# Performance work log

Hardware: AMD Instinct MI355X
Metric: run time of the kernel (lower is better)

The kernel has to match this reference:

```python
import jax, jax.numpy as jnp
import numpy as np

B, S, D, H = 2, 4096, 512, 8
DK = D // H


def setup_inputs() -> dict:
    key = jax.random.key(0)
    ks = jax.random.split(key, 8)
    q = jax.random.normal(ks[0], (B, S, D), dtype=jnp.float32)
    k = jax.random.normal(ks[1], (B, S, D), dtype=jnp.float32)
    v = jax.random.normal(ks[2], (B, S, D), dtype=jnp.float32)
    mask = jax.random.randint(ks[3], (B, S, S), 0, 2, dtype=jnp.int32)
    scale = 1.0 / np.sqrt(D)
    w_q = jax.random.normal(ks[4], (D, D), dtype=jnp.float32) * scale
    w_k = jax.random.normal(ks[5], (D, D), dtype=jnp.float32) * scale
    w_v = jax.random.normal(ks[6], (D, D), dtype=jnp.float32) * scale
    w_o = jax.random.normal(ks[7], (D, D), dtype=jnp.float32) * scale
    return {"q": q, "k": k, "v": v, "mask": mask,
            "w_q": w_q, "w_k": w_k, "w_v": w_v, "w_o": w_o}


def reference(q, k, v, mask, w_q, w_k, w_v, w_o):
    # Projections (weights stored as [in, out]; no bias, matching bias=False)
    # [B,S,D] -> [B,H,S,DK]
    def split_heads(x):
        return x.reshape(B, S, H, DK).transpose(0, 2, 1, 3)

    qh = split_heads(q @ w_q)
    kh = split_heads(k @ w_k)
    vh = split_heads(v @ w_v)

    inv_sqrt_dk = jnp.float32(1.0 / np.sqrt(DK))
    # Explicit O(S^2) score matrix, as in the original module
    scores = jnp.einsum('bhqd,bhkd->bhqk', qh, kh) * inv_sqrt_dk
    scores = jnp.where(mask[:, None, :, :] == 0, jnp.float32(-1e9), scores)
    attn = jax.nn.softmax(scores, axis=-1)
    # dropout in eval mode (p=0) -> identity
    x = jnp.einsum('bhqk,bhkd->bhqd', attn, vh)
    x = x.transpose(0, 2, 1, 3).reshape(B, S, D)
    return x @ w_o
```

## Files before the change

kernel.cpp:

```cpp
#include <hip/hip_runtime.h>
#include <hip/hip_bf16.h>

#define Bn 2
#define Sn 4096
#define Dn 512
#define Hn 8
#define DKn 64

typedef __attribute__((ext_vector_type(8))) short bf16x8;
typedef __attribute__((ext_vector_type(4))) float f32x4;
typedef __attribute__((ext_vector_type(4))) _Float16 f16x4;
typedef __attribute__((ext_vector_type(8))) unsigned short us8;
typedef __attribute__((ext_vector_type(4))) unsigned short us4;

__device__ __forceinline__ unsigned short f2bf(float f) {
  unsigned u = __builtin_bit_cast(unsigned, f);
  u += 0x7fffu + ((u >> 16) & 1u);
  return (unsigned short)(u >> 16);
}

__global__ __launch_bounds__(256) void pack_mask_k(const int* __restrict__ mask,
                                                   unsigned int* __restrict__ pm) {
  int gid = blockIdx.x * 256 + threadIdx.x;
  int m = mask[gid];
  unsigned long long bal = __ballot(m != 0);
  if ((threadIdx.x & 63) == 0) {
    int q = (gid >> 12) & 4095;
    int b = gid >> 24;
    int kvw = (gid >> 5) & 127;
    pm[((size_t)b * 128 + kvw) * 4096 + q] = (unsigned)bal;
    pm[((size_t)b * 128 + kvw + 1) * 4096 + q] = (unsigned)(bal >> 32);
  }
}

__global__ __launch_bounds__(256) void cvt_k(const float* __restrict__ q,
                                             const float* __restrict__ k,
                                             const float* __restrict__ v,
                                             unsigned short* __restrict__ o) {
  const float* src = blockIdx.y == 0 ? q : blockIdx.y == 1 ? k : v;
  size_t i = (size_t)blockIdx.x * 256 + threadIdx.x;
  float4 f = *(const float4*)&src[i * 4];
  us4 r = {f2bf(f.x), f2bf(f.y), f2bf(f.z), f2bf(f.w)};
  *(us4*)&o[(size_t)blockIdx.y * (Bn * Sn * Dn) + i * 4] = r;
}

__global__ __launch_bounds__(256) void wt_k(const float* __restrict__ wq,
                                            const float* __restrict__ wk,
                                            const float* __restrict__ wv,
                                            const float* __restrict__ wo,
                                            unsigned short* __restrict__ wt) {
  __shared__ unsigned short ls[64][68];
  const float* W = blockIdx.z == 0 ? wq : blockIdx.z == 1 ? wk
                 : blockIdx.z == 2 ? wv : wo;
  int k0 = blockIdx.x * 64, n0 = blockIdx.y * 64;
  int t = threadIdx.x;
  for (int j = 0; j < 4; ++j) {
    int i = t + j * 256;
    int r = i >> 4, c4 = (i & 15) << 2;
    float4 f = *(const float4*)&W[(size_t)(k0 + r) * 512 + n0 + c4];
    ls[c4 + 0][r] = f2bf(f.x);
    ls[c4 + 1][r] = f2bf(f.y);
    ls[c4 + 2][r] = f2bf(f.z);
    ls[c4 + 3][r] = f2bf(f.w);
  }
  __syncthreads();
  unsigned short* out = wt + (size_t)blockIdx.z * 512 * 512;
  for (int j = 0; j < 4; ++j) {
    int i = t + j * 256;
    int r = i >> 4, c4 = (i & 15) << 2;
    us4 v = {ls[r][c4], ls[r][c4 + 1], ls[r][c4 + 2], ls[r][c4 + 3]};
    *(us4*)&out[(size_t)(n0 + r) * 512 + k0 + c4] = v;
  }
}

template <int MT, bool HEADS>
__global__ __launch_bounds__(256, 2) void gemm_k(
    const unsigned short* __restrict__ A0, size_t zstride,
    const unsigned short* __restrict__ wt, unsigned short* __restrict__ oh,
    unsigned short* __restrict__ vtg, float* __restrict__ olin) {
  __shared__ unsigned short smem[MT * 8192 + 16384];
  const int z = blockIdx.z;
  const unsigned short* A = A0 + zstride * z;
  const unsigned short* Wt = wt + (size_t)z * 512 * 512;
  const float scale = (HEADS && z == 0) ? 0.125f * 1.44269504088896f : 1.0f;
  const int m0 = blockIdx.x * (MT * 64), n0 = blockIdx.y * 128;
  const int t = threadIdx.x, w = t >> 6, l = t & 63;
  const int quad = l >> 4, c = l & 15;

  f32x4 acc[MT][8] = {};
  us8 apre[MT * 2], bpre[4];

#pragma unroll
  for (int j = 0; j < MT * 2; ++j) {
    int i = t + j * 256, r = i >> 3, u = i & 7;
    apre[j] = *(const us8*)&A[(size_t)(m0 + r) * 512 + (u << 3)];
  }
#pragma unroll
  for (int j = 0; j < 4; ++j) {
    int i = t + j * 256, r = i >> 3, u = i & 7;
    bpre[j] = *(const us8*)&Wt[(size_t)(n0 + r) * 512 + (u << 3)];
  }
#pragma unroll
  for (int j = 0; j < MT * 2; ++j) {
    int i = t + j * 256, r = i >> 3, u = i & 7;
    *(us8*)&smem[r * 64 + ((u ^ (r & 7)) << 3)] = apre[j];
  }
#pragma unroll
  for (int j = 0; j < 4; ++j) {
    int i = t + j * 256, r = i >> 3, u = i & 7;
    *(us8*)&smem[MT * 8192 + r * 64 + ((u ^ (r & 7)) << 3)] = bpre[j];
  }

  for (int k0 = 0; k0 < 512; k0 += 64) {
    const int cur = (k0 >> 6) & 1;
    const unsigned short* AsC = &smem[cur * (MT * 4096)];
    const unsigned short* BsC = &smem[MT * 8192 + cur * 8192];
    __syncthreads();
    const bool nxt = k0 + 64 < 512;
    if (nxt) {
#pragma unroll
      for (int j = 0; j < MT * 2; ++j) {
        int i = t + j * 256, r = i >> 3, u = i & 7;
        apre[j] = *(const us8*)&A[(size_t)(m0 + r) * 512 + k0 + 64 + (u << 3)];
      }
#pragma unroll
      for (int j = 0; j < 4; ++j) {
        int i = t + j * 256, r = i >> 3, u = i & 7;
        bpre[j] = *(const us8*)&Wt[(size_t)(n0 + r) * 512 + k0 + 64 + (u << 3)];
      }
    }

#pragma unroll
    for (int kc = 0; kc < 2; ++kc) {
      bf16x8 aA[MT], bB[8];
      int u = kc * 4 + quad;
#pragma unroll
      for (int mt = 0; mt < MT; ++mt) {
        int row = w * (MT * 16) + mt * 16 + c;
        aA[mt] = *(const bf16x8*)&AsC[row * 64 + ((u ^ (c & 7)) << 3)];
      }
#pragma unroll
      for (int nt = 0; nt < 8; ++nt) {
        int row = nt * 16 + c;
        bB[nt] = *(const bf16x8*)&BsC[row * 64 + ((u ^ (c & 7)) << 3)];
      }
#pragma unroll
      for (int mt = 0; mt < MT; ++mt)
#pragma unroll
        for (int nt = 0; nt < 8; ++nt)
          acc[mt][nt] = __builtin_amdgcn_mfma_f32_16x16x32_bf16(
              aA[mt], bB[nt], acc[mt][nt], 0, 0, 0);
    }

    if (nxt) {
      unsigned short* AsN = &smem[(cur ^ 1) * (MT * 4096)];
      unsigned short* BsN = &smem[MT * 8192 + (cur ^ 1) * 8192];
#pragma unroll
      for (int j = 0; j < MT * 2; ++j) {
        int i = t + j * 256, r = i >> 3, u = i & 7;
        *(us8*)&AsN[r * 64 + ((u ^ (r & 7)) << 3)] = apre[j];
      }
#pragma unroll
      for (int j = 0; j < 4; ++j) {
        int i = t + j * 256, r = i >> 3, u = i & 7;
        *(us8*)&BsN[r * 64 + ((u ^ (r & 7)) << 3)] = bpre[j];
      }
    }
  }

  if constexpr (HEADS) {
    if (z == 2) {
      __syncthreads();
#pragma unroll
      for (int mt = 0; mt < MT; ++mt) {
        int mb = w * (MT * 16) + mt * 16 + (quad << 2);
        int ml = (mb & 64) | (((mb >> 5) & 1) << 5) | (((mb >> 2) & 3) << 3) |
                 (((mb >> 4) & 1) << 2);
#pragma unroll
        for (int nt = 0; nt < 8; ++nt) {
          int nl = nt * 16 + c;
          us4 pk;
#pragma unroll
          for (int r = 0; r < 4; ++r)
            pk[r] = __builtin_bit_cast(unsigned short, (_Float16)acc[mt][nt][r]);
          *(us4*)&smem[nl * 152 + ml] = pk;
        }
      }
      __syncthreads();
      const int bb = m0 >> 12, sb = m0 & 4095;
#pragma unroll
      for (int j = 0; j < MT * 4; ++j) {
        int i = t + j * 256;
        int nl = i >> 4, mc = (i & 15) << 3;
        us8 vv = *(const us8*)&smem[nl * 152 + mc];
        int n = n0 + nl, hh = n >> 6, dk = n & 63;
        *(us8*)&vtg[((size_t)(bb * Hn + hh) * DKn + dk) * Sn + sb + mc] = vv;
      }
    } else {
#pragma unroll
      for (int mt = 0; mt < MT; ++mt)
#pragma unroll
        for (int nt = 0; nt < 8; ++nt)
#pragma unroll
          for (int r = 0; r < 4; ++r) {
            int m = m0 + w * (MT * 16) + mt * 16 + (quad << 2) + r;
            int n = n0 + nt * 16 + c;
            int b = m >> 12, s = m & 4095, hh = n >> 6, dk = n & 63;
            oh[(size_t)z * (Bn * Hn * Sn * DKn) +
               ((size_t)(b * Hn + hh) * Sn + s) * DKn + dk] =
                f2bf(acc[mt][nt][r] * scale);
          }
    }
  } else {
#pragma unroll
    for (int mt = 0; mt < MT; ++mt)
#pragma unroll
      for (int nt = 0; nt < 8; ++nt)
#pragma unroll
        for (int r = 0; r < 4; ++r) {
          int m = m0 + w * (MT * 16) + mt * 16 + (quad << 2) + r;
          int n = n0 + nt * 16 + c;
          olin[(size_t)m * 512 + n] = acc[mt][nt][r];
        }
  }
}

__global__ __launch_bounds__(256, 2) void flash_k(
    const unsigned short* __restrict__ Qh, const unsigned short* __restrict__ Kh,
    const unsigned short* __restrict__ VtG, const unsigned int* __restrict__ pmt,
    unsigned short* __restrict__ attn) {
  __shared__ unsigned short Ks[2][64 * 64];
  __shared__ unsigned short Vts[2][64 * 64];
  __shared__ unsigned int Mw[2][256];

  const int q0 = blockIdx.x * 128, h = blockIdx.y, b = blockIdx.z;
  const int t = threadIdx.x, w = t >> 6, l = t & 63;
  const int quad = l >> 4, c = l & 15;
  const size_t hb = (size_t)(b * Hn + h) * Sn * DKn;
  const unsigned short* Qg = Qh + hb;
  const unsigned short* Kg = Kh + hb;
  const unsigned short* Vg = VtG + hb;

  bf16x8 bQ[2][2];
#pragma unroll
  for (int qf = 0; qf < 2; ++qf) {
    int qrow = q0 + w * 32 + qf * 16 + c;
#pragma unroll
    for (int kc = 0; kc < 2; ++kc)
      bQ[qf][kc] = *(const bf16x8*)&Qg[(size_t)qrow * 64 + kc * 32 + quad * 8];
  }

  f32x4 oacc[2][4] = {};
  float lsum[2] = {};
  const int sr = t >> 3, su = t & 7;
  const int off0 = sr * 64 + ((su ^ (sr & 7)) << 3);
  const int off1 = (sr + 32) * 64 + ((su ^ (sr & 7)) << 3);

  us8 kpre[2], vpre[2];
  unsigned mpre;
  kpre[0] = *(const us8*)&Kg[(size_t)sr * 64 + (su << 3)];
  kpre[1] = *(const us8*)&Kg[(size_t)(sr + 32) * 64 + (su << 3)];
  vpre[0] = *(const us8*)&Vg[(size_t)sr * Sn + (su << 3)];
  vpre[1] = *(const us8*)&Vg[(size_t)(sr + 32) * Sn + (su << 3)];
  mpre = pmt[((size_t)b * 128 + (t >> 7)) * 4096 + q0 + (t & 127)];
  *(us8*)&Ks[0][off0] = kpre[0];
  *(us8*)&Ks[0][off1] = kpre[1];
  *(us8*)&Vts[0][off0] = vpre[0];
  *(us8*)&Vts[0][off1] = vpre[1];
  Mw[0][t] = mpre;

  for (int kv0 = 0; kv0 < Sn; kv0 += 64) {
    const int cur = (kv0 >> 6) & 1;
    __syncthreads();
    const bool nxt = kv0 + 64 < Sn;
    if (nxt) {
      kpre[0] = *(const us8*)&Kg[(size_t)(kv0 + 64 + sr) * 64 + (su << 3)];
      kpre[1] = *(const us8*)&Kg[(size_t)(kv0 + 96 + sr) * 64 + (su << 3)];
      vpre[0] = *(const us8*)&Vg[(size_t)sr * Sn + kv0 + 64 + (su << 3)];
      vpre[1] = *(const us8*)&Vg[(size_t)(sr + 32) * Sn + kv0 + 64 + (su << 3)];
      mpre = pmt[((size_t)b * 128 + ((kv0 + 64) >> 5) + (t >> 7)) * 4096 +
                 q0 + (t & 127)];
    }

    f32x4 sacc[2][4] = {};
#pragma unroll
    for (int kc = 0; kc < 2; ++kc) {
      int u = kc * 4 + quad;
#pragma unroll
      for (int kvt = 0; kvt < 4; ++kvt) {
        int row = kvt * 16 + c;
        bf16x8 aK = *(const bf16x8*)&Ks[cur][row * 64 + ((u ^ (c & 7)) << 3)];
#pragma unroll
        for (int qf = 0; qf < 2; ++qf)
          sacc[qf][kvt] = __builtin_amdgcn_mfma_f32_16x16x32_bf16(
              aK, bQ[qf][kc], sacc[qf][kvt], 0, 0, 0);
      }
    }

    f16x4 pb[2][4];
#pragma unroll
    for (int qf = 0; qf < 2; ++qf) {
      int qloc = w * 32 + qf * 16 + c;
      unsigned mv0 = Mw[cur][qloc], mv1 = Mw[cur][128 + qloc];
#pragma unroll
      for (int kvt = 0; kvt < 4; ++kvt) {
        unsigned word = (kvt & 2) ? mv1 : mv0;
        unsigned bits = (word >> (((kvt & 1) << 4) + (quad << 2))) & 15u;
        float ps = 0.f;
#pragma unroll
        for (int r = 0; r < 4; ++r) {
          float p = ((bits >> r) & 1u) ? __builtin_amdgcn_exp2f(sacc[qf][kvt][r])
                                       : 0.f;
          ps += p;
          pb[qf][kvt][r] = (_Float16)p;
        }
        lsum[qf] += ps;
      }
    }

#pragma unroll
    for (int kp = 0; kp < 2; ++kp) {
#pragma unroll
      for (int dkt = 0; dkt < 4; ++dkt) {
        int dk = dkt * 16 + c;
        us8 vv = *(const us8*)&Vts[cur][dk * 64 +
                                        (((kp * 4 + quad) ^ (c & 7)) << 3)];
        f16x4 lo = __builtin_bit_cast(f16x4, (us4){vv[0], vv[1], vv[2], vv[3]});
        f16x4 hi = __builtin_bit_cast(f16x4, (us4){vv[4], vv[5], vv[6], vv[7]});
#pragma unroll
        for (int qf = 0; qf < 2; ++qf) {
          oacc[qf][dkt] = __builtin_amdgcn_mfma_f32_16x16x16f16(
              pb[qf][kp * 2], lo, oacc[qf][dkt], 0, 0, 0);
          oacc[qf][dkt] = __builtin_amdgcn_mfma_f32_16x16x16f16(
              pb[qf][kp * 2 + 1], hi, oacc[qf][dkt], 0, 0, 0);
        }
      }
    }

    if (nxt) {
      const int nb = cur ^ 1;
      *(us8*)&Ks[nb][off0] = kpre[0];
      *(us8*)&Ks[nb][off1] = kpre[1];
      *(us8*)&Vts[nb][off0] = vpre[0];
      *(us8*)&Vts[nb][off1] = vpre[1];
      Mw[nb][t] = mpre;
    }
  }

#pragma unroll
  for (int qf = 0; qf < 2; ++qf) {
    float s = lsum[qf];
    s += __shfl_xor(s, 16, 64);
    s += __shfl_xor(s, 32, 64);
    float inv = 1.0f / s;
#pragma unroll
    for (int r = 0; r < 4; ++r) {
      float invr = __shfl(inv, (quad << 2) + r, 64);
      unsigned short* dst =
          &attn[((size_t)(b * Sn + q0 + w * 32 + qf * 16 + (quad << 2) + r)) * Dn +
                h * 64 + c];
#pragma unroll
      for (int dkt = 0; dkt < 4; ++dkt)
        dst[dkt * 16] = f2bf(oacc[qf][dkt][r] * invr);
    }
  }
}

extern "C" void kernel_launch(void* const* d_in, const int* in_sizes, int n_in,
                              void* d_out, int out_size, void* d_ws,
                              size_t ws_size, hipStream_t stream) {
  const float* q = (const float*)d_in[0];
  const float* k = (const float*)d_in[1];
  const float* v = (const float*)d_in[2];
  const int* mask = (const int*)d_in[3];
  const float* wq = (const float*)d_in[4];
  const float* wk = (const float*)d_in[5];
  const float* wv = (const float*)d_in[6];
  const float* wo = (const float*)d_in[7];
  float* out = (float*)d_out;

  char* ws = (char*)d_ws;
  const size_t headN = (size_t)Bn * Hn * Sn * DKn;
  const size_t tensB = headN * 2;
  unsigned short* qbkb = (unsigned short*)ws;
  unsigned short* attn = (unsigned short*)ws;
  size_t off = 3 * tensB;
  unsigned short* qkv = (unsigned short*)(ws + off);
  off += 3 * tensB;
  unsigned short* wt = (unsigned short*)(ws + off);
  off += 4ull * 512 * 512 * 2;
  unsigned int* pm = (unsigned int*)(ws + off);

  pack_mask_k<<<(Bn * Sn * Sn) / 256, 256, 0, stream>>>(mask, pm);
  cvt_k<<<dim3(4096, 3), 256, 0, stream>>>(q, k, v, qbkb);
  wt_k<<<dim3(8, 8, 4), 256, 0, stream>>>(wq, wk, wv, wo, wt);
  gemm_k<2, true><<<dim3(64, 4, 3), 256, 0, stream>>>(
      qbkb, headN, wt, qkv, qkv + 2 * headN, nullptr);
  flash_k<<<dim3(32, 8, 2), 256, 0, stream>>>(qkv, qkv + headN,
                                              qkv + 2 * headN, pm, attn);
  gemm_k<1, false><<<dim3(128, 4, 1), 256, 0, stream>>>(
      attn, 0, wt + 3ull * 512 * 512, nullptr, nullptr, out);
}
```

Before: 409.4 us.

## Split KV range across two warp groups in flash kernel and merge partials

Doubles the flash attention block to 512 threads, with two 256-thread groups each handling alternate 64-wide KV tiles in their own double-buffered shared memory. After the loop, the partial outputs and row sums are reduced through shared memory. The change also swaps the 16x16x16 f16 MFMA pairs for the 16x16x32 f16 instruction, and uses packed cvt_pkrtz plus fdot2 for the softmax sums. This aims to raise occupancy with only 512 blocks per launch (two groups per block), at the cost of a shared-memory reduction, more LDS per block and higher register pressure under launch bounds of 512 threads and 4 blocks.

```diff
diff --git a/kernel.cpp b/kernel.cpp
--- a/kernel.cpp
+++ b/kernel.cpp
@@ -10,6 +10,8 @@
 typedef __attribute__((ext_vector_type(8))) short bf16x8;
 typedef __attribute__((ext_vector_type(4))) float f32x4;
 typedef __attribute__((ext_vector_type(4))) _Float16 f16x4;
+typedef __attribute__((ext_vector_type(8))) _Float16 f16x8;
+typedef __attribute__((ext_vector_type(2))) _Float16 f16x2;
 typedef __attribute__((ext_vector_type(8))) unsigned short us8;
 typedef __attribute__((ext_vector_type(4))) unsigned short us4;
 
@@ -225,16 +227,18 @@
   }
 }
 
-__global__ __launch_bounds__(256, 2) void flash_k(
+__global__ __launch_bounds__(512, 4) void flash_k(
     const unsigned short* __restrict__ Qh, const unsigned short* __restrict__ Kh,
     const unsigned short* __restrict__ VtG, const unsigned int* __restrict__ pmt,
     unsigned short* __restrict__ attn) {
-  __shared__ unsigned short Ks[2][64 * 64];
-  __shared__ unsigned short Vts[2][64 * 64];
-  __shared__ unsigned int Mw[2][256];
+  __shared__ unsigned short Ks[2][2][64 * 64];
+  __shared__ unsigned short Vts[2][2][64 * 64];
+  __shared__ unsigned int Mw[2][2][256];
 
   const int q0 = blockIdx.x * 128, h = blockIdx.y, b = blockIdx.z;
-  const int t = threadIdx.x, w = t >> 6, l = t & 63;
+  const int t = threadIdx.x;
+  const int g = t >> 8, tg = t & 255;
+  const int w = (t >> 6) & 3, l = t & 63;
   const int quad = l >> 4, c = l & 15;
   const size_t hb = (size_t)(b * Hn + h) * Sn * DKn;
   const unsigned short* Qg = Qh + hb;
@@ -252,34 +256,38 @@
 
   f32x4 oacc[2][4] = {};
   float lsum[2] = {};
-  const int sr = t >> 3, su = t & 7;
+  const int sr = tg >> 3, su = tg & 7;
   const int off0 = sr * 64 + ((su ^ (sr & 7)) << 3);
   const int off1 = (sr + 32) * 64 + ((su ^ (sr & 7)) << 3);
+  const f16x2 one2 = {(_Float16)1.0f, (_Float16)1.0f};
 
   us8 kpre[2], vpre[2];
   unsigned mpre;
-  kpre[0] = *(const us8*)&Kg[(size_t)sr * 64 + (su << 3)];
-  kpre[1] = *(const us8*)&Kg[(size_t)(sr + 32) * 64 + (su << 3)];
-  vpre[0] = *(const us8*)&Vg[(size_t)sr * Sn + (su << 3)];
-  vpre[1] = *(const us8*)&Vg[(size_t)(sr + 32) * Sn + (su << 3)];
-  mpre = pmt[((size_t)b * 128 + (t >> 7)) * 4096 + q0 + (t & 127)];
-  *(us8*)&Ks[0][off0] = kpre[0];
-  *(us8*)&Ks[0][off1] = kpre[1];
-  *(us8*)&Vts[0][off0] = vpre[0];
-  *(us8*)&Vts[0][off1] = vpre[1];
-  Mw[0][t] = mpre;
-
-  for (int kv0 = 0; kv0 < Sn; kv0 += 64) {
-    const int cur = (kv0 >> 6) & 1;
+  {
+    const int kvF = g * 64;
+    kpre[0] = *(const us8*)&Kg[(size_t)(kvF + sr) * 64 + (su << 3)];
+    kpre[1] = *(const us8*)&Kg[(size_t)(kvF + sr + 32) * 64 + (su << 3)];
+    vpre[0] = *(const us8*)&Vg[(size_t)sr * Sn + kvF + (su << 3)];
+    vpre[1] = *(const us8*)&Vg[(size_t)(sr + 32) * Sn + kvF + (su << 3)];
+    mpre = pmt[((size_t)b * 128 + (kvF >> 5) + (tg >> 7)) * 4096 + q0 + (tg & 127)];
+    *(us8*)&Ks[g][0][off0] = kpre[0];
+    *(us8*)&Ks[g][0][off1] = kpre[1];
+    *(us8*)&Vts[g][0][off0] = vpre[0];
+    *(us8*)&Vts[g][0][off1] = vpre[1];
+    Mw[g][0][tg] = mpre;
+  }
+
+  for (int it = 0; it < 32; ++it) {
+    const int cur = it & 1;
     __syncthreads();
-    const bool nxt = kv0 + 64 < Sn;
+    const bool nxt = it + 1 < 32;
     if (nxt) {
-      kpre[0] = *(const us8*)&Kg[(size_t)(kv0 + 64 + sr) * 64 + (su << 3)];
-      kpre[1] = *(const us8*)&Kg[(size_t)(kv0 + 96 + sr) * 64 + (su << 3)];
-      vpre[0] = *(const us8*)&Vg[(size_t)sr * Sn + kv0 + 64 + (su << 3)];
-      vpre[1] = *(const us8*)&Vg[(size_t)(sr + 32) * Sn + kv0 + 64 + (su << 3)];
-      mpre = pmt[((size_t)b * 128 + ((kv0 + 64) >> 5) + (t >> 7)) * 4096 +
-                 q0 + (t & 127)];
+      const int kvN = (2 * (it + 1) + g) * 64;
+      kpre[0] = *(const us8*)&Kg[(size_t)(kvN + sr) * 64 + (su << 3)];
+      kpre[1] = *(const us8*)&Kg[(size_t)(kvN + sr + 32) * 64 + (su << 3)];
+      vpre[0] = *(const us8*)&Vg[(size_t)sr * Sn + kvN + (su << 3)];
+      vpre[1] = *(const us8*)&Vg[(size_t)(sr + 32) * Sn + kvN + (su << 3)];
+      mpre = pmt[((size_t)b * 128 + (kvN >> 5) + (tg >> 7)) * 4096 + q0 + (tg & 127)];
     }
 
     f32x4 sacc[2][4] = {};
@@ -289,7 +297,7 @@
 #pragma unroll
       for (int kvt = 0; kvt < 4; ++kvt) {
         int row = kvt * 16 + c;
-        bf16x8 aK = *(const bf16x8*)&Ks[cur][row * 64 + ((u ^ (c & 7)) << 3)];
+        bf16x8 aK = *(const bf16x8*)&Ks[g][cur][row * 64 + ((u ^ (c & 7)) << 3)];
 #pragma unroll
         for (int qf = 0; qf < 2; ++qf)
           sacc[qf][kvt] = __builtin_amdgcn_mfma_f32_16x16x32_bf16(
@@ -297,71 +305,99 @@
       }
     }
 
-    f16x4 pb[2][4];
+    f16x8 ph[2][2];
 #pragma unroll
     for (int qf = 0; qf < 2; ++qf) {
       int qloc = w * 32 + qf * 16 + c;
-      unsigned mv0 = Mw[cur][qloc], mv1 = Mw[cur][128 + qloc];
-#pragma unroll
-      for (int kvt = 0; kvt < 4; ++kvt) {
-        unsigned word = (kvt & 2) ? mv1 : mv0;
-        unsigned bits = (word >> (((kvt & 1) << 4) + (quad << 2))) & 15u;
-        float ps = 0.f;
-#pragma unroll
-        for (int r = 0; r < 4; ++r) {
-          float p = ((bits >> r) & 1u) ? __builtin_amdgcn_exp2f(sacc[qf][kvt][r])
-                                       : 0.f;
-          ps += p;
-          pb[qf][kvt][r] = (_Float16)p;
+      unsigned mv0 = Mw[g][cur][qloc], mv1 = Mw[g][cur][128 + qloc];
+#pragma unroll
+      for (int half = 0; half < 2; ++half) {
+        unsigned word = half ? mv1 : mv0;
+        uint4 ww;
+#pragma unroll
+        for (int kvh = 0; kvh < 2; ++kvh) {
+          unsigned bits = (word >> ((kvh << 4) + (quad << 2))) & 15u;
+          const f32x4 s4 = sacc[qf][half * 2 + kvh];
+          float p0 = (bits & 1u) ? __builtin_amdgcn_exp2f(s4[0]) : 0.f;
+          float p1 = (bits & 2u) ? __builtin_amdgcn_exp2f(s4[1]) : 0.f;
+          float p2 = (bits & 4u) ? __builtin_amdgcn_exp2f(s4[2]) : 0.f;
+          float p3 = (bits & 8u) ? __builtin_amdgcn_exp2f(s4[3]) : 0.f;
+          f16x2 a = __builtin_bit_cast(f16x2, __builtin_amdgcn_cvt_pkrtz(p0, p1));
+          f16x2 bpk = __builtin_bit_cast(f16x2, __builtin_amdgcn_cvt_pkrtz(p2, p3));
+          lsum[qf] = __builtin_amdgcn_fdot2(a, one2, lsum[qf], false);
+          lsum[qf] = __builtin_amdgcn_fdot2(bpk, one2, lsum[qf], false);
+          (&ww.x)[kvh * 2] = __builtin_bit_cast(unsigned, a);
+          (&ww.x)[kvh * 2 + 1] = __builtin_bit_cast(unsigned, bpk);
         }
-        lsum[qf] += ps;
-      }
-    }
-
-#pragma unroll
-    for (int kp = 0; kp < 2; ++kp) {
+        ph[qf][half] = __builtin_bit_cast(f16x8, ww);
+      }
+    }
+
+#pragma unroll
+    for (int half = 0; half < 2; ++half) {
+      int u2 = half * 4 + quad;
 #pragma unroll
       for (int dkt = 0; dkt < 4; ++dkt) {
         int dk = dkt * 16 + c;
-        us8 vv = *(const us8*)&Vts[cur][dk * 64 +
-                                        (((kp * 4 + quad) ^ (c & 7)) << 3)];
-        f16x4 lo = __builtin_bit_cast(f16x4, (us4){vv[0], vv[1], vv[2], vv[3]});
-        f16x4 hi = __builtin_bit_cast(f16x4, (us4){vv[4], vv[5], vv[6], vv[7]});
-#pragma unroll
-        for (int qf = 0; qf < 2; ++qf) {
-          oacc[qf][dkt] = __builtin_amdgcn_mfma_f32_16x16x16f16(
-              pb[qf][kp * 2], lo, oacc[qf][dkt], 0, 0, 0);
-          oacc[qf][dkt] = __builtin_amdgcn_mfma_f32_16x16x16f16(
-              pb[qf][kp * 2 + 1], hi, oacc[qf][dkt], 0, 0, 0);
-        }
+        f16x8 bV = __builtin_bit_cast(
+            f16x8, *(const us8*)&Vts[g][cur][dk * 64 + ((u2 ^ (c & 7)) << 3)]);
+#pragma unroll
+        for (int qf = 0; qf < 2; ++qf)
+          oacc[qf][dkt] = __builtin_amdgcn_mfma_f32_16x16x32_f16(
+              ph[qf][half], bV, oacc[qf][dkt], 0, 0, 0);
       }
     }
 
     if (nxt) {
       const int nb = cur ^ 1;
-      *(us8*)&Ks[nb][off0] = kpre[0];
-      *(us8*)&Ks[nb][off1] = kpre[1];
-      *(us8*)&Vts[nb][off0] = vpre[0];
-      *(us8*)&Vts[nb][off1] = vpre[1];
-      Mw[nb][t] = mpre;
-    }
-  }
-
-#pragma unroll
-  for (int qf = 0; qf < 2; ++qf) {
-    float s = lsum[qf];
-    s += __shfl_xor(s, 16, 64);
-    s += __shfl_xor(s, 32, 64);
-    float inv = 1.0f / s;
-#pragma unroll
-    for (int r = 0; r < 4; ++r) {
-      float invr = __shfl(inv, (quad << 2) + r, 64);
-      unsigned short* dst =
-          &attn[((size_t)(b * Sn + q0 + w * 32 + qf * 16 + (quad << 2) + r)) * Dn +
-                h * 64 + c];
+      *(us8*)&Ks[g][nb][off0] = kpre[0];
+      *(us8*)&Ks[g][nb][off1] = kpre[1];
+      *(us8*)&Vts[g][nb][off0] = vpre[0];
+      *(us8*)&Vts[g][nb][off1] = vpre[1];
+      Mw[g][nb][tg] = mpre;
+    }
+  }
+
+  __syncthreads();
+  float* fsum = (float*)&Ks[0][0][0];
+  float* flsum = (float*)&Vts[0][0][0];
+  if (g == 1) {
+#pragma unroll
+    for (int qf = 0; qf < 2; ++qf) {
 #pragma unroll
       for (int dkt = 0; dkt < 4; ++dkt)
-        dst[dkt * 16] = f2bf(oacc[qf][dkt][r] * invr);
+        *(f32x4*)&fsum[(((qf * 4 + dkt) * 4 + w) * 64 + l) * 4] = oacc[qf][dkt];
+      flsum[(qf * 4 + w) * 64 + l] = lsum[qf];
+    }
+  }
+  __syncthreads();
+  if (g == 0) {
+#pragma unroll
+    for (int qf = 0; qf < 2; ++qf) {
+      lsum[qf] += flsum[(qf * 4 + w) * 64 + l];
+#pragma unroll
+      for (int dkt = 0; dkt < 4; ++dkt) {
+        f32x4 o1 = *(const f32x4*)&fsum[(((qf * 4 + dkt) * 4 + w) * 64 + l) * 4];
+#pragma unroll
+        for (int r = 0; r < 4; ++r) oacc[qf][dkt][r] += o1[r];
+      }
+    }
+#pragma unroll
+    for (int qf = 0; qf < 2; ++qf) {
+      float s = lsum[qf];
+      s += __shfl_xor(s, 16, 64);
+      s += __shfl_xor(s, 32, 64);
+      float inv = 1.0f / s;
+#pragma unroll
+      for (int r = 0; r < 4; ++r) {
+        float invr = __shfl(inv, (quad << 2) + r, 64);
+        unsigned short* dst =
+            &attn[((size_t)(b * Sn + q0 + w * 32 + qf * 16 + (quad << 2) + r)) * Dn +
+                  h * 64 + c];
+#pragma unroll
+        for (int dkt = 0; dkt < 4; ++dkt)
+          dst[dkt * 16] = f2bf(oacc[qf][dkt][r] * invr);
+      }
     }
   }
 }
@@ -396,7 +432,7 @@
   wt_k<<<dim3(8, 8, 4), 256, 0, stream>>>(wq, wk, wv, wo, wt);
   gemm_k<2, true><<<dim3(64, 4, 3), 256, 0, stream>>>(
       qbkb, headN, wt, qkv, qkv + 2 * headN, nullptr);
-  flash_k<<<dim3(32, 8, 2), 256, 0, stream>>>(qkv, qkv + headN,
+  flash_k<<<dim3(32, 8, 2), 512, 0, stream>>>(qkv, qkv + headN,
                                               qkv + 2 * headN, pm, attn);
   gemm_k<1, false><<<dim3(128, 4, 1), 256, 0, stream>>>(
       attn, 0, wt + 3ull * 512 * 512, nullptr, nullptr, out);
```

Result: faster. 388.2 us (-5.2%).
